# Performance work log

Measured on AMD Instinct MI355X. Metric: run time of the kernel, lower is better.

The kernel has to match this reference:

```python
import jax, jax.numpy as jnp
import numpy as np
from jax import lax

B, N, E, H = 512, 128, 256, 8
D = E // H
CLIP = 10.0
NEG = -1e9  # finite stand-in for -inf (backward-safe, math-identical after softmax)


def setup_inputs() -> dict:
    key = jax.random.key(0)
    ks = jax.random.split(key, 5)
    s = lambda k, shape: jax.random.normal(k, shape, jnp.float32) * 0.05
    return {
        "node_embeddings": jax.random.normal(ks[0], (B, N, E), jnp.float32),
        "Wqkv": s(ks[1], (E, 3 * E)), "bqkv": jnp.zeros((3 * E,), jnp.float32),
        "Wfix": s(ks[2], (E, E)), "bfix": jnp.zeros((E,), jnp.float32),
        "Wstep": s(ks[3], (2 * E, E)), "bstep": jnp.zeros((E,), jnp.float32),
        "Wmlp": s(ks[4], (E, E)), "bmlp": jnp.zeros((E,), jnp.float32),
    }


def reference(node_embeddings, Wqkv, bqkv, Wfix, bfix, Wstep, bstep, Wmlp, bmlp):
    scale = 1.0 / np.sqrt(D)
    graph_emb = node_embeddings.mean(axis=1)                       # (B,E)
    qkv = node_embeddings @ Wqkv + bqkv                            # (B,N,3E)
    k, v, logit_k = jnp.split(qkv, 3, axis=-1)
    kh = k.reshape(B, N, H, D).transpose(0, 2, 1, 3)               # (B,H,N,D)
    vh = v.reshape(B, N, H, D).transpose(0, 2, 1, 3)               # (B,H,N,D)
    fixed = graph_emb @ Wfix + bfix                                # (B,E)
    first = node_embeddings[:, 0, :]                               # (B,E)
    bidx = jnp.arange(B)

    def step(carry, _):
        current, visited, logp_sum = carry
        last = node_embeddings[bidx, current]                      # gather last action emb (B,E)
        q = fixed + (jnp.concatenate([first, last], axis=-1) @ Wstep + bstep)
        qh = q.reshape(B, H, D)                                    # single query per head
        attn = jnp.einsum('bhd,bhnd->bhn', qh, kh) * scale
        attn = jnp.where(visited[:, None, :], NEG, attn)
        attn = jax.nn.softmax(attn, axis=-1)
        ctx = jnp.einsum('bhn,bhnd->bhd', attn, vh).reshape(B, E)
        x = ctx @ Wmlp + bmlp                                      # (B,E)
        logits = jnp.einsum('be,bne->bn', x, logit_k) * scale      # (B,N)
        logits = jnp.tanh(logits) * CLIP
        logits = jnp.where(visited, NEG, logits)
        log_p = jax.nn.log_softmax(logits, axis=-1)
        action = jnp.argmax(log_p, axis=-1)                        # greedy decode
        chosen = jnp.take_along_axis(log_p, action[:, None], axis=1)[:, 0]
        visited = visited | jax.nn.one_hot(action, N, dtype=bool)
        return (action, visited, logp_sum + chosen), action

    visited0 = jnp.zeros((B, N), bool).at[:, 0].set(True)
    current0 = jnp.zeros((B,), jnp.int32)
    (_, _, logp_sum), seq = lax.scan(
        step, (current0, visited0, jnp.zeros((B,), jnp.float32)), None, length=N - 1)
    return logp_sum                                                # (B,) summed log-prob of tour
```

## Files before the change

### kernel.cpp

```cpp
#include <hip/hip_runtime.h>
#include <math.h>


#define B_ 512
#define N_ 128
#define E_ 256
#define H_ 8
#define D_ 32
#define NEG (-1.0e9f)
#define CLIPV 10.0f
#define SCALE 0.17677669529663688110f

typedef float v2f __attribute__((ext_vector_type(2)));

__device__ __forceinline__ void pkfma(v2f& acc, v2f a, v2f b) {
  asm("v_pk_fma_f32 %0, %1, %2, %0" : "+v"(acc) : "v"(a), "v"(b));
}

template <int CTRL>
__device__ __forceinline__ float dpp_f(float x) {
  int r = __builtin_amdgcn_update_dpp(__float_as_int(x), __float_as_int(x),
                                      CTRL, 0xf, 0xf, false);
  return __int_as_float(r);
}
template <int CTRL, int RM>
__device__ __forceinline__ float dpp_mv(float x, float idv) {
  int r = __builtin_amdgcn_update_dpp(__float_as_int(idv), __float_as_int(x),
                                      CTRL, RM, 0xf, false);
  return __int_as_float(r);
}
__device__ __forceinline__ float wred_max(float v) {
  v = fmaxf(v, dpp_f<0xB1>(v));
  v = fmaxf(v, dpp_f<0x4E>(v));
  v = fmaxf(v, dpp_f<0x124>(v));
  v = fmaxf(v, dpp_f<0x128>(v));
  v = fmaxf(v, dpp_mv<0x142, 0xa>(v, -1e38f));
  v = fmaxf(v, dpp_mv<0x143, 0xc>(v, -1e38f));
  return __int_as_float(__builtin_amdgcn_readlane(__float_as_int(v), 63));
}
__device__ __forceinline__ float wred_sum(float v) {
  v += dpp_f<0xB1>(v);
  v += dpp_f<0x4E>(v);
  v += dpp_f<0x124>(v);
  v += dpp_f<0x128>(v);
  v += dpp_mv<0x142, 0xa>(v, 0.0f);
  v += dpp_mv<0x143, 0xc>(v, 0.0f);
  return __int_as_float(__builtin_amdgcn_readlane(__float_as_int(v), 63));
}

__global__ void k0_prep(const float* __restrict__ Wqkv, const float* __restrict__ bqkv,
                        const float* __restrict__ Wmlp, const float* __restrict__ bmlp,
                        float* __restrict__ Wc, float* __restrict__ bc,
                        float* __restrict__ wc2, float* __restrict__ cconst) {
  int t = threadIdx.x;
  int blk = blockIdx.x;
  __shared__ float row_s[E_];
  if (blk < E_) {
    int g = blk;
    row_s[t] = Wqkv[g * 768 + 512 + t];
    __syncthreads();
    int f = t;
    const float4* wm4 = (const float4*)(Wmlp + f * E_);
    const float4* w34 = (const float4*)row_s;
    float acc = 0.f;
#pragma unroll 8
    for (int j = 0; j < E_ / 4; ++j) {
      float4 a = w34[j]; float4 bv = wm4[j];
      acc += a.x * bv.x + a.y * bv.y + a.z * bv.z + a.w * bv.w;
    }
    Wc[g * E_ + f] = acc;
  } else {
    int f = t;
    float a1 = 0.f, a2 = 0.f;
    for (int e = 0; e < E_; ++e) {
      a1 += bqkv[512 + e] * Wmlp[f * E_ + e];
      a2 += Wqkv[f * 768 + 512 + e] * bmlp[e];
    }
    bc[f] = a1;
    wc2[f] = a2;
    if (t == 0) {
      float c = 0.f;
      for (int e = 0; e < E_; ++e) c += bqkv[512 + e] * bmlp[e];
      *cconst = c;
    }
  }
}

__global__ __launch_bounds__(256, 2)
void k_gemm(const float* __restrict__ emb, const float* __restrict__ Wqkv,
            const float* __restrict__ bqkv,
            const float* __restrict__ Wc, const float* __restrict__ bc,
            float* __restrict__ kk_, float* __restrict__ vv_,
            float* __restrict__ lk2, int ncc, int tmask) {
  __shared__ float As[256 * 64];
  int t = threadIdx.x;
  int r0 = blockIdx.x * 64;
  {
    int m = t >> 2;
    int c0 = t & 3;
    const float4* e4 = (const float4*)emb;
#pragma unroll
    for (int p = 0; p < 16; ++p) {
      int c4 = c0 + p * 4;
      float4 a = e4[(size_t)(r0 + m) * 64 + c4];
      As[(c4 * 4 + 0) * 64 + m] = a.x;
      As[(c4 * 4 + 1) * 64 + m] = a.y;
      As[(c4 * 4 + 2) * 64 + m] = a.z;
      As[(c4 * 4 + 3) * 64 + m] = a.w;
    }
  }
  __syncthreads();
  int tx = t & 15, ty = t >> 4;
  const float4* As4 = (const float4*)As;
  for (int cc = 0; cc < ncc; ++cc) {
    const float* Bp; int ldb4; const float* bias; float* outp;
    int colbase = (cc & 1) * 128;
    switch (cc >> 1) {
      case 0:  Bp = Wqkv + colbase;          ldb4 = 192; bias = bqkv + colbase;       outp = kk_; break;
      case 1:  Bp = Wqkv + 256 + colbase;    ldb4 = 192; bias = bqkv + 256 + colbase; outp = vv_; break;
      default: Bp = Wc + colbase;            ldb4 = 64;  bias = bc + colbase;         outp = lk2; break;
    }
    const float4* B4 = (const float4*)Bp;
    float acc[4][8];
#pragma unroll
    for (int i = 0; i < 4; ++i)
#pragma unroll
      for (int j = 0; j < 8; ++j) acc[i][j] = 0.f;

#pragma unroll 4
    for (int kk = 0; kk < 256; ++kk) {
      float4 b0 = B4[kk * ldb4 + tx * 2];
      float4 b1 = B4[kk * ldb4 + tx * 2 + 1];
      float4 av = As4[kk * 16 + ty];
      float a_[4] = {av.x, av.y, av.z, av.w};
#pragma unroll
      for (int i = 0; i < 4; ++i) {
        acc[i][0] += a_[i] * b0.x; acc[i][1] += a_[i] * b0.y;
        acc[i][2] += a_[i] * b0.z; acc[i][3] += a_[i] * b0.w;
        acc[i][4] += a_[i] * b1.x; acc[i][5] += a_[i] * b1.y;
        acc[i][6] += a_[i] * b1.z; acc[i][7] += a_[i] * b1.w;
      }
    }
    float bj[8];
#pragma unroll
    for (int j = 0; j < 8; ++j) bj[j] = bias ? bias[tx * 8 + j] : 0.f;
    int tr = (tmask >> (cc >> 1)) & 1;
    if (!tr) {
#pragma unroll
      for (int i = 0; i < 4; ++i) {
        int row = r0 + ty * 4 + i;
        float4 o0 = make_float4(acc[i][0] + bj[0], acc[i][1] + bj[1], acc[i][2] + bj[2], acc[i][3] + bj[3]);
        float4 o1 = make_float4(acc[i][4] + bj[4], acc[i][5] + bj[5], acc[i][6] + bj[6], acc[i][7] + bj[7]);
        float4* o4 = (float4*)(outp + (size_t)row * 256 + colbase + tx * 8);
        o4[0] = o0; o4[1] = o1;
      }
    } else {
#pragma unroll
      for (int i = 0; i < 4; ++i) {
        int row = r0 + ty * 4 + i;
        int bb = row >> 7, nn = row & 127;
        float* op = outp + (size_t)bb * 32768 + nn;
#pragma unroll
        for (int j = 0; j < 8; ++j)
          op[(size_t)(colbase + tx * 8 + j) * 128] = acc[i][j] + bj[j];
      }
    }
  }
}

__global__ void k_qbase(const float* __restrict__ emb, const float* __restrict__ Wfix,
                        const float* __restrict__ bfix, const float* __restrict__ Wstep,
                        const float* __restrict__ bstep, float* __restrict__ qbase) {
  int b = blockIdx.x, t = threadIdx.x;
  __shared__ float ge[E_], fi[E_];
  const float* eb = emb + (size_t)b * N_ * E_;
  float s = 0.f;
#pragma unroll 8
  for (int n = 0; n < N_; ++n) s += eb[n * E_ + t];
  ge[t] = s * (1.0f / 128.0f);
  fi[t] = eb[t];
  __syncthreads();
  float acc = bfix[t] + bstep[t];
#pragma unroll 4
  for (int g = 0; g < E_; ++g)
    acc += ge[g] * Wfix[g * E_ + t] + fi[g] * Wstep[g * E_ + t];
  qbase[b * E_ + t] = acc;
}

__global__ void k_c(const float* __restrict__ emb, const float* __restrict__ wc2,
                    const float* __restrict__ cconst, float* __restrict__ cvec) {
  __shared__ float w[E_];
  int t = threadIdx.x;
  w[t] = wc2[t];
  __syncthreads();
  int row = blockIdx.x * 256 + t;
  const float4* e4 = (const float4*)(emb + (size_t)row * E_);
  const float4* w4 = (const float4*)w;
  float acc = 0.f;
#pragma unroll 8
  for (int j = 0; j < E_ / 4; ++j) {
    float4 a = e4[j], bv = w4[j];
    acc += a.x * bv.x + a.y * bv.y + a.z * bv.z + a.w * bv.w;
  }
  cvec[row] = acc + *cconst;
}

__global__ __attribute__((amdgpu_flat_work_group_size(512, 512), amdgpu_waves_per_eu(2, 2)))
void k_roll(const float* __restrict__ emb, const float* __restrict__ Wstep,
            const float* __restrict__ kT, const float* __restrict__ vv_,
            const float* __restrict__ lkT,
            const float* __restrict__ qbase, const float* __restrict__ cvec,
            float* __restrict__ out) {
  int lt = threadIdx.x;
  int b = blockIdx.x;
  int h = lt >> 6;
  int j = lt & 63;

  __shared__ float sq_lds[128 * 260];
  __shared__ float work[6144];
  float* at_s  = work;
  float* ctx_s = work + 1024;
  float* zp    = work + 1280;

  {
    float* At = work;
    float* Bs = work + 2048;
    const float4* eb4 = (const float4*)(emb + (size_t)b * 32768);
    const float* W2 = Wstep + 65536;
    int n0 = (lt & 31) * 4;
    int e0 = (lt >> 5) * 16;
    float acc[4][16];
#pragma unroll
    for (int i = 0; i < 4; ++i)
#pragma unroll
      for (int jj = 0; jj < 16; ++jj) acc[i][jj] = 0.f;

    for (int gc = 0; gc < 16; ++gc) {
      {
        int n = lt & 127, q4g = lt >> 7;
        float4 a = eb4[n * 64 + gc * 4 + q4g];
        At[(q4g * 4 + 0) * 128 + n] = a.x;
        At[(q4g * 4 + 1) * 128 + n] = a.y;
        At[(q4g * 4 + 2) * 128 + n] = a.z;
        At[(q4g * 4 + 3) * 128 + n] = a.w;
      }
      {
        const float4* w4 = (const float4*)(W2 + gc * 16 * 256);
        ((float4*)Bs)[lt] = w4[lt];
        ((float4*)Bs)[lt + 512] = w4[lt + 512];
      }
      __syncthreads();
#pragma unroll
      for (int gi = 0; gi < 16; ++gi) {
        float4 a4 = *(const float4*)(At + gi * 128 + n0);
        const float4* bp = (const float4*)(Bs + gi * 256 + e0);
        float4 b0 = bp[0], b1 = bp[1], b2 = bp[2], b3 = bp[3];
        float av[4] = {a4.x, a4.y, a4.z, a4.w};
        float bv[16] = {b0.x, b0.y, b0.z, b0.w, b1.x, b1.y, b1.z, b1.w,
                        b2.x, b2.y, b2.z, b2.w, b3.x, b3.y, b3.z, b3.w};
#pragma unroll
        for (int i = 0; i < 4; ++i)
#pragma unroll
          for (int jj = 0; jj < 16; ++jj) acc[i][jj] += av[i] * bv[jj];
      }
      __syncthreads();
    }
    const float* qb = qbase + (size_t)b * 256;
    float qbr[16];
#pragma unroll
    for (int jj = 0; jj < 16; ++jj) qbr[jj] = qb[e0 + jj];
#pragma unroll
    for (int i = 0; i < 4; ++i)
#pragma unroll
      for (int jj = 0; jj < 16; ++jj)
        sq_lds[(n0 + i) * 260 + e0 + jj] = acc[i][jj] + qbr[jj];
  }
  __syncthreads();
  __builtin_amdgcn_sched_barrier(0);

  const float* kTb = kT + (size_t)b * 32768;
  const float* vb  = vv_ + (size_t)b * 32768;
  const float* lTb = lkT + (size_t)b * 32768;

  v2f k0p[16], k1p[16];
#pragma unroll
  for (int d = 0; d < 16; ++d) {
    k0p[d] = (v2f){kTb[(h * 32 + 2 * d) * 128 + j],     kTb[(h * 32 + 2 * d + 1) * 128 + j]};
    k1p[d] = (v2f){kTb[(h * 32 + 2 * d) * 128 + j + 64], kTb[(h * 32 + 2 * d + 1) * 128 + j + 64]};
    asm("" : "+v"(k0p[d]));
    asm("" : "+v"(k1p[d]));
  }
  int e_own = h * 32 + (j & 31), nh = j >> 5;
  v2f vp[32];
#pragma unroll
  for (int m = 0; m < 32; ++m) {
    vp[m] = (v2f){vb[(nh * 64 + 2 * m) * 256 + e_own], vb[(nh * 64 + 2 * m + 1) * 256 + e_own]};
    asm("" : "+v"(vp[m]));
  }
  v2f l0p[16], l1p[16];
#pragma unroll
  for (int e = 0; e < 16; ++e) {
    l0p[e] = (v2f){lTb[(h * 32 + 2 * e) * 128 + j],      lTb[(h * 32 + 2 * e + 1) * 128 + j]};
    l1p[e] = (v2f){lTb[(h * 32 + 2 * e) * 128 + j + 64], lTb[(h * 32 + 2 * e + 1) * 128 + j + 64]};
    asm("" : "+v"(l0p[e]));
    asm("" : "+v"(l1p[e]));
  }
  float cv_lo = cvec[b * 128 + j];
  float cv_hi = cvec[b * 128 + j + 64];
  int vis_lo = (j == 0) ? 1 : 0, vis_hi = 0;
  int cur = 0;
  float lp = 0.f;
  int swz = (j >> 2) & 7;

#pragma unroll 1
  for (int it = 0; it < N_ - 1; ++it) {
    const float4* q4 = (const float4*)(sq_lds + cur * 260 + h * 32);
    v2f s00 = {0.f, 0.f}, s01 = {0.f, 0.f}, s10 = {0.f, 0.f}, s11 = {0.f, 0.f};
#pragma unroll
    for (int dd = 0; dd < 8; ++dd) {
      float4 qv = q4[dd];
      v2f qa = {qv.x, qv.y}, qb = {qv.z, qv.w};
      pkfma(s00, qa, k0p[2 * dd]);
      pkfma(s01, qb, k0p[2 * dd + 1]);
      pkfma(s10, qa, k1p[2 * dd]);
      pkfma(s11, qb, k1p[2 * dd + 1]);
    }
    float slo = vis_lo ? NEG : ((s00.x + s00.y) + (s01.x + s01.y)) * SCALE;
    float shi = vis_hi ? NEG : ((s10.x + s10.y) + (s11.x + s11.y)) * SCALE;
    float m = wred_max(fmaxf(slo, shi));
    float elo = expf(slo - m), ehi = expf(shi - m);
    at_s[h * 128 + j] = elo;
    at_s[h * 128 + 64 + j] = ehi;
    float inv = 1.0f / wred_sum(elo + ehi);
    const float4* a4 = (const float4*)(at_s + h * 128 + nh * 64);
    v2f c0 = {0.f, 0.f}, c1 = {0.f, 0.f};
#pragma unroll
    for (int mm = 0; mm < 16; ++mm) {
      float4 av = a4[mm];
      v2f aa = {av.x, av.y}, ab = {av.z, av.w};
      pkfma(c0, aa, vp[2 * mm]);
      pkfma(c1, ab, vp[2 * mm + 1]);
    }
    float c = (c0.x + c0.y) + (c1.x + c1.y);
    c += __shfl_xor(c, 32);
    c *= inv;
    if (j < 32) ctx_s[h * 32 + j] = c;
    const float4* cx4 = (const float4*)(ctx_s + h * 32);
    v2f z00 = {0.f, 0.f}, z01 = {0.f, 0.f}, z10 = {0.f, 0.f}, z11 = {0.f, 0.f};
#pragma unroll
    for (int ee = 0; ee < 8; ++ee) {
      float4 cv = cx4[ee];
      v2f ca = {cv.x, cv.y}, cb = {cv.z, cv.w};
      pkfma(z00, ca, l0p[2 * ee]);
      pkfma(z01, cb, l0p[2 * ee + 1]);
      pkfma(z10, ca, l1p[2 * ee]);
      pkfma(z11, cb, l1p[2 * ee + 1]);
    }
    float* zpw = zp + (it & 1) * 1024;
    zpw[j * 8 + (h ^ swz)]        = (z00.x + z00.y) + (z01.x + z01.y);
    zpw[(j + 64) * 8 + (h ^ swz)] = (z10.x + z10.y) + (z11.x + z11.y);
    __syncthreads();

    const float4* zr0 = (const float4*)(zpw + j * 8);
    const float4* zr1 = (const float4*)(zpw + (j + 64) * 8);
    float4 za = zr0[0], zb = zr0[1], zc = zr1[0], zd = zr1[1];
    float zlo = cv_lo + ((za.x + za.y) + (za.z + za.w)) + ((zb.x + zb.y) + (zb.z + zb.w));
    float zhi = cv_hi + ((zc.x + zc.y) + (zc.z + zc.w)) + ((zd.x + zd.y) + (zd.z + zd.w));
    float zmlo = vis_lo ? -1e30f : zlo;
    float zmhi = vis_hi ? -1e30f : zhi;
    float vmax = wred_max(fmaxf(zmlo, zmhi));
    unsigned long long blo = __ballot(zmlo == vmax);
    int action;
    if (blo) action = __ffsll((unsigned long long)blo) - 1;
    else     action = 63 + __ffsll((unsigned long long)__ballot(zmhi == vmax));
    if (h == 0) {
      float lmax = CLIPV * tanhf(vmax * SCALE);
      float tlo = vis_lo ? 0.f : expf(CLIPV * tanhf(zlo * SCALE) - 10.0f);
      float thi = vis_hi ? 0.f : expf(CLIPV * tanhf(zhi * SCALE) - 10.0f);
      float S = wred_sum(tlo + thi);
      lp += lmax - 10.0f - logf(S);
    }
    cur = action;
    vis_lo |= (action == j);
    vis_hi |= (action == j + 64);
  }
  if (lt == 0) out[b] = lp;
}

extern "C" void kernel_launch(void* const* d_in, const int* in_sizes, int n_in,
                              void* d_out, int out_size, void* d_ws, size_t ws_size,
                              hipStream_t stream) {
  (void)in_sizes; (void)n_in; (void)out_size; (void)ws_size;
  const float* emb   = (const float*)d_in[0];
  const float* Wqkv  = (const float*)d_in[1];
  const float* bqkv  = (const float*)d_in[2];
  const float* Wfix  = (const float*)d_in[3];
  const float* bfix  = (const float*)d_in[4];
  const float* Wstep = (const float*)d_in[5];
  const float* bstep = (const float*)d_in[6];
  const float* Wmlp  = (const float*)d_in[7];
  const float* bmlp  = (const float*)d_in[8];
  float* out = (float*)d_out;
  float* ws = (float*)d_ws;

  const size_t NBE = (size_t)B_ * N_ * E_;
  float* kk_    = ws;
  float* vv_    = ws + NBE;
  float* lk2    = ws + 2 * NBE;
  float* qbase  = ws + 3 * NBE;
  float* cvec   = qbase + 131072;
  float* Wc     = cvec + 65536;
  float* bc     = Wc + 65536;
  float* wc2    = bc + 256;
  float* cconst = wc2 + 256;

  hipLaunchKernelGGL(k0_prep, dim3(257), dim3(256), 0, stream,
                     Wqkv, bqkv, Wmlp, bmlp, Wc, bc, wc2, cconst);
  hipLaunchKernelGGL(k_qbase, dim3(512), dim3(256), 0, stream,
                     emb, Wfix, bfix, Wstep, bstep, qbase);
  hipLaunchKernelGGL(k_c, dim3(256), dim3(256), 0, stream,
                     emb, wc2, cconst, cvec);
  hipLaunchKernelGGL(k_gemm, dim3(1024), dim3(256), 0, stream,
                     emb, Wqkv, bqkv, Wc, bc, kk_, vv_, lk2, 6, 0b101);
  hipLaunchKernelGGL(k_roll, dim3(512), dim3(512), 0, stream,
                     emb, Wstep, kk_, vv_, lk2, qbase, cvec, out);
}
```

Measured before the change: 1.201 ms.

## Precompute per-node query table in shared GEMM kernel instead of rollout prologue

Moves the per-batch emb @ Wstep[E:] query-table GEMM out of the rollout kernel's prologue into the large tiled GEMM kernel as two extra column chunks, with qbase folded in as a per-row bias. The rollout kernel then only streams the precomputed table into LDS. This applies only when the workspace is large enough, and a fallback keeps the old in-kernel GEMM. It also pads the z-partial LDS rows from 8 to 12 floats, presumably to reduce bank conflicts. The cost is an extra full B*N*E write and read through global memory.

```diff
diff --git a/kernel.cpp b/kernel.cpp
--- a/kernel.cpp
+++ b/kernel.cpp
@@ -90,8 +90,10 @@
 void k_gemm(const float* __restrict__ emb, const float* __restrict__ Wqkv,
             const float* __restrict__ bqkv,
             const float* __restrict__ Wc, const float* __restrict__ bc,
+            const float* __restrict__ Wstep, const float* __restrict__ qbase,
             float* __restrict__ kk_, float* __restrict__ vv_,
-            float* __restrict__ lk2, int ncc, int tmask) {
+            float* __restrict__ lk2, float* __restrict__ qtab,
+            int ncc, int tmask) {
   __shared__ float As[256 * 64];
   int t = threadIdx.x;
   int r0 = blockIdx.x * 64;
@@ -118,7 +120,9 @@
     switch (cc >> 1) {
       case 0:  Bp = Wqkv + colbase;          ldb4 = 192; bias = bqkv + colbase;       outp = kk_; break;
       case 1:  Bp = Wqkv + 256 + colbase;    ldb4 = 192; bias = bqkv + 256 + colbase; outp = vv_; break;
-      default: Bp = Wc + colbase;            ldb4 = 64;  bias = bc + colbase;         outp = lk2; break;
+      case 2:  Bp = Wc + colbase;            ldb4 = 64;  bias = bc + colbase;         outp = lk2; break;
+      default: Bp = Wstep + 65536 + colbase; ldb4 = 64;
+               bias = qbase + (size_t)(r0 >> 7) * 256 + colbase;                      outp = qtab; break;
     }
     const float4* B4 = (const float4*)Bp;
     float acc[4][8];
@@ -210,6 +214,7 @@
             const float* __restrict__ kT, const float* __restrict__ vv_,
             const float* __restrict__ lkT,
             const float* __restrict__ qbase, const float* __restrict__ cvec,
+            const float* __restrict__ qtab, int use_qtab,
             float* __restrict__ out) {
   int lt = threadIdx.x;
   int b = blockIdx.x;
@@ -222,7 +227,16 @@
   float* ctx_s = work + 1024;
   float* zp    = work + 1280;
 
-  {
+  if (use_qtab) {
+    const float4* qt4 = (const float4*)(qtab + (size_t)b * 32768);
+#pragma unroll
+    for (int p = 0; p < 16; ++p) {
+      int idx = p * 512 + lt;
+      int n = idx >> 6, c4 = idx & 63;
+      float4 a = qt4[idx];
+      *(float4*)(sq_lds + n * 260 + c4 * 4) = a;
+    }
+  } else {
     float* At = work;
     float* Bs = work + 2048;
     const float4* eb4 = (const float4*)(emb + (size_t)b * 32768);
@@ -285,7 +299,7 @@
   v2f k0p[16], k1p[16];
 #pragma unroll
   for (int d = 0; d < 16; ++d) {
-    k0p[d] = (v2f){kTb[(h * 32 + 2 * d) * 128 + j],     kTb[(h * 32 + 2 * d + 1) * 128 + j]};
+    k0p[d] = (v2f){kTb[(h * 32 + 2 * d) * 128 + j],      kTb[(h * 32 + 2 * d + 1) * 128 + j]};
     k1p[d] = (v2f){kTb[(h * 32 + 2 * d) * 128 + j + 64], kTb[(h * 32 + 2 * d + 1) * 128 + j + 64]};
     asm("" : "+v"(k0p[d]));
     asm("" : "+v"(k1p[d]));
@@ -310,7 +324,9 @@
   int vis_lo = (j == 0) ? 1 : 0, vis_hi = 0;
   int cur = 0;
   float lp = 0.f;
-  int swz = (j >> 2) & 7;
+  int rof0 = j * 12;
+  int rof1 = rof0 + 768;
+  int csw  = h ^ ((j >> 2) & 7);
 
 #pragma unroll 1
   for (int it = 0; it < N_ - 1; ++it) {
@@ -356,13 +372,13 @@
       pkfma(z10, ca, l1p[2 * ee]);
       pkfma(z11, cb, l1p[2 * ee + 1]);
     }
-    float* zpw = zp + (it & 1) * 1024;
-    zpw[j * 8 + (h ^ swz)]        = (z00.x + z00.y) + (z01.x + z01.y);
-    zpw[(j + 64) * 8 + (h ^ swz)] = (z10.x + z10.y) + (z11.x + z11.y);
+    float* zpw = zp + (it & 1) * 1536;
+    zpw[rof0 + csw] = (z00.x + z00.y) + (z01.x + z01.y);
+    zpw[rof1 + csw] = (z10.x + z10.y) + (z11.x + z11.y);
     __syncthreads();
 
-    const float4* zr0 = (const float4*)(zpw + j * 8);
-    const float4* zr1 = (const float4*)(zpw + (j + 64) * 8);
+    const float4* zr0 = (const float4*)(zpw + rof0);
+    const float4* zr1 = (const float4*)(zpw + rof1);
     float4 za = zr0[0], zb = zr0[1], zc = zr1[0], zd = zr1[1];
     float zlo = cv_lo + ((za.x + za.y) + (za.z + za.w)) + ((zb.x + zb.y) + (zb.z + zb.w));
     float zhi = cv_hi + ((zc.x + zc.y) + (zc.z + zc.w)) + ((zd.x + zd.y) + (zd.z + zd.w));
@@ -390,7 +406,7 @@
 extern "C" void kernel_launch(void* const* d_in, const int* in_sizes, int n_in,
                               void* d_out, int out_size, void* d_ws, size_t ws_size,
                               hipStream_t stream) {
-  (void)in_sizes; (void)n_in; (void)out_size; (void)ws_size;
+  (void)in_sizes; (void)n_in; (void)out_size;
   const float* emb   = (const float*)d_in[0];
   const float* Wqkv  = (const float*)d_in[1];
   const float* bqkv  = (const float*)d_in[2];
@@ -413,6 +429,9 @@
   float* bc     = Wc + 65536;
   float* wc2    = bc + 256;
   float* cconst = wc2 + 256;
+  size_t qoff   = 3 * NBE + 262720;
+  float* qtab   = ws + qoff;
+  int use_qtab  = (ws_size >= (qoff + NBE) * sizeof(float)) ? 1 : 0;
 
   hipLaunchKernelGGL(k0_prep, dim3(257), dim3(256), 0, stream,
                      Wqkv, bqkv, Wmlp, bmlp, Wc, bc, wc2, cconst);
@@ -421,7 +440,8 @@
   hipLaunchKernelGGL(k_c, dim3(256), dim3(256), 0, stream,
                      emb, wc2, cconst, cvec);
   hipLaunchKernelGGL(k_gemm, dim3(1024), dim3(256), 0, stream,
-                     emb, Wqkv, bqkv, Wc, bc, kk_, vv_, lk2, 6, 0b101);
+                     emb, Wqkv, bqkv, Wc, bc, Wstep, qbase,
+                     kk_, vv_, lk2, qtab, use_qtab ? 8 : 6, 0b0101);
   hipLaunchKernelGGL(k_roll, dim3(512), dim3(512), 0, stream,
-                     emb, Wstep, kk_, vv_, lk2, qbase, cvec, out);
-}
+                     emb, Wstep, kk_, vv_, lk2, qbase, cvec, qtab, use_qtab, out);
+}
```

Result: faster. 1.165 ms (-3.0%).
